# Kernel optimization log

Measured on AMD Instinct MI355X. Metric: run time of the kernel, lower is better.

## Reference

```python
import jax, jax.numpy as jnp
import numpy as np

BS, N, HEADS, DIN, DOUT = 512, 128, 8, 64, 64


def setup_inputs() -> dict:
    key = jax.random.key(0)
    k1, k2, k3, k4, k5 = jax.random.split(key, 5)
    h = jax.random.normal(k1, (BS, N, DIN), dtype=jnp.float32)
    w = jax.random.normal(k2, (HEADS, DIN, DOUT), dtype=jnp.float32) * 0.1
    a_src = jax.random.normal(k3, (HEADS, DOUT, 1), dtype=jnp.float32) * 0.1
    a_dst = jax.random.normal(k4, (HEADS, DOUT, 1), dtype=jnp.float32) * 0.1
    bias = jnp.zeros((DOUT,), dtype=jnp.float32)
    # sparse random adjacency with self-loops so every softmax row is valid
    adj = jax.random.uniform(k5, (BS, N, N)) < 0.05
    adj = adj | jnp.eye(N, dtype=bool)[None, :, :]
    return {"h": h, "adj": adj, "w": w, "a_src": a_src, "a_dst": a_dst, "bias": bias}


def reference(h, adj, w, a_src, a_dst, bias):
    # h: [b, n, i]; w: [H, i, o] -> h_prime: [b, H, n, o]
    h_prime = jnp.einsum('bni,hio->bhno', h, w)
    t = jnp.tanh(h_prime)
    attn_src = jnp.einsum('bhno,ho->bhn', t, a_src[..., 0])  # [b, H, n]
    attn_dst = jnp.einsum('bhno,ho->bhn', t, a_dst[..., 0])  # [b, H, n]
    # attn[b,h,i,j] = src[b,h,i] + dst[b,h,j]
    attn = attn_src[..., :, None] + attn_dst[..., None, :]
    attn = jax.nn.leaky_relu(attn, negative_slope=0.2)
    attn = jnp.where(adj[:, None, :, :], attn, -jnp.inf)
    attn = jax.nn.softmax(attn, axis=-1)
    out = jnp.einsum('bhij,bhjo->bhio', attn, h_prime)
    return out + bias
```

## Files before the change

### kernel.cpp

```cpp
#include <hip/hip_runtime.h>

#define BSZ 512
#define NN 128
#define HEADS 8
#define DIN 64
#define DOUT 64

typedef __bf16 bf16x8 __attribute__((ext_vector_type(8)));
typedef float floatx4 __attribute__((ext_vector_type(4)));

static __device__ __forceinline__ unsigned short f2bf(float f) {
    __bf16 b = (__bf16)f;
    return __builtin_bit_cast(unsigned short, b);
}
static __device__ __forceinline__ bf16x8 ld_frag(const unsigned short* p) {
    uint4 r = *reinterpret_cast<const uint4*>(p);
    return __builtin_bit_cast(bf16x8, r);
}

__global__ __launch_bounds__(512) void prep(
    const int* __restrict__ adj, const float* __restrict__ w,
    unsigned int* __restrict__ msk, unsigned short* __restrict__ wT, int do_w)
{
    const int b = blockIdx.x;
    const int t = threadIdx.x;
    const int* ap = adj + (size_t)b * NN * NN + (t >> 2) * NN + (t & 3) * 32;
    unsigned int m = 0;
    #pragma unroll
    for (int q = 0; q < 8; ++q) {
        int4 v = *reinterpret_cast<const int4*>(ap + q * 4);
        m |= (v.x != 0 ? (1u << (4 * q + 0)) : 0u)
           | (v.y != 0 ? (1u << (4 * q + 1)) : 0u)
           | (v.z != 0 ? (1u << (4 * q + 2)) : 0u)
           | (v.w != 0 ? (1u << (4 * q + 3)) : 0u);
    }
    msk[b * 512 + t] = m;

    if (do_w && b < HEADS) {
        const float* wg = w + b * DIN * DOUT;
        const int o = t >> 3, k0 = (t & 7) * 8;
        unsigned int u[4];
        #pragma unroll
        for (int p = 0; p < 4; ++p) {
            float f0 = wg[(k0 + 2 * p) * DOUT + o];
            float f1 = wg[(k0 + 2 * p + 1) * DOUT + o];
            u[p] = f2bf(f0) | ((unsigned int)f2bf(f1) << 16);
        }
        *reinterpret_cast<uint4*>(&wT[b * DOUT * DIN + o * DIN + k0]) =
            make_uint4(u[0], u[1], u[2], u[3]);
    }
}

__global__ __launch_bounds__(512, 8) void gat_fwd(
    const float* __restrict__ hin,
    const unsigned int* __restrict__ mskg,
    const unsigned short* __restrict__ wTg,
    const float* __restrict__ w,
    const float* __restrict__ a_src,
    const float* __restrict__ a_dst,
    const float* __restrict__ bias,
    float* __restrict__ out)
{
    __shared__ __attribute__((aligned(16))) unsigned short hpT[DOUT * NN];
    __shared__ __attribute__((aligned(16))) float s_src[NN];
    __shared__ __attribute__((aligned(16))) float s_dst[NN];

    const int bid  = blockIdx.x;
    const int b    = bid >> 3;
    const int hd   = bid & 7;
    const int tid  = threadIdx.x;
    const int lane = tid & 63;
    const int wv   = tid >> 6;
    const int lg   = lane >> 4;
    const int lm   = lane & 15;
    const int n0   = wv * 16;

    const float* hb = hin + (size_t)b * NN * DIN;
    bf16x8 hA[2];
    #pragma unroll
    for (int kt = 0; kt < 2; ++kt) {
        const float* p = hb + (n0 + lm) * DIN + kt * 32 + lg * 8;
        float4 v0 = *reinterpret_cast<const float4*>(p);
        float4 v1 = *reinterpret_cast<const float4*>(p + 4);
        bf16x8 a;
        a[0] = (__bf16)v0.x; a[1] = (__bf16)v0.y; a[2] = (__bf16)v0.z; a[3] = (__bf16)v0.w;
        a[4] = (__bf16)v1.x; a[5] = (__bf16)v1.y; a[6] = (__bf16)v1.z; a[7] = (__bf16)v1.w;
        hA[kt] = a;
    }
    const uint4 mr = *reinterpret_cast<const uint4*>(&mskg[(size_t)b * 512 + (n0 + lm) * 4]);
    unsigned int mwv[4] = {mr.x, mr.y, mr.z, mr.w};

    floatx4 acc[4] = {floatx4{0,0,0,0}, floatx4{0,0,0,0}, floatx4{0,0,0,0}, floatx4{0,0,0,0}};
    if (wTg) {
        const unsigned short* wt = wTg + hd * DOUT * DIN;
        #pragma unroll
        for (int kt = 0; kt < 2; ++kt) {
            #pragma unroll
            for (int nt = 0; nt < 4; ++nt) {
                bf16x8 bfr = ld_frag(&wt[(nt * 16 + lm) * DIN + kt * 32 + lg * 8]);
                acc[nt] = __builtin_amdgcn_mfma_f32_16x16x32_bf16(hA[kt], bfr, acc[nt], 0, 0, 0);
            }
        }
    } else {
        const float* wg = w + hd * DIN * DOUT;
        #pragma unroll
        for (int kt = 0; kt < 2; ++kt) {
            #pragma unroll
            for (int nt = 0; nt < 4; ++nt) {
                const float* wp = wg + (kt * 32 + lg * 8) * DOUT + nt * 16 + lm;
                bf16x8 bfr;
                #pragma unroll
                for (int q = 0; q < 8; ++q) bfr[q] = (__bf16)wp[q * DOUT];
                acc[nt] = __builtin_amdgcn_mfma_f32_16x16x32_bf16(hA[kt], bfr, acc[nt], 0, 0, 0);
            }
        }
    }
    const float* asp = a_src + hd * DOUT;
    const float* adp = a_dst + hd * DOUT;
    float ps[4] = {0, 0, 0, 0}, pd[4] = {0, 0, 0, 0};
    #pragma unroll
    for (int nt = 0; nt < 4; ++nt) {
        const int o = nt * 16 + lm;
        const float as = asp[o], ad = adp[o];
        #pragma unroll
        for (int r = 0; r < 4; ++r) {
            const float v = acc[nt][r];
            const float ex = __expf(2.f * v);
            const float t = 1.f - 2.f / (ex + 1.f);
            ps[r] = fmaf(t, as, ps[r]);
            pd[r] = fmaf(t, ad, pd[r]);
        }
        const int jb = n0 + lg * 4;
        unsigned int u01 = f2bf(acc[nt][0]) | ((unsigned int)f2bf(acc[nt][1]) << 16);
        unsigned int u23 = f2bf(acc[nt][2]) | ((unsigned int)f2bf(acc[nt][3]) << 16);
        const int base = (o * 128 + jb) ^ ((o & 7) << 3);
        *reinterpret_cast<unsigned int*>(&hpT[base])     = u01;
        *reinterpret_cast<unsigned int*>(&hpT[base + 2]) = u23;
    }
    #pragma unroll
    for (int r = 0; r < 4; ++r) {
        #pragma unroll
        for (int m = 1; m <= 8; m <<= 1) {
            ps[r] += __shfl_xor(ps[r], m);
            pd[r] += __shfl_xor(pd[r], m);
        }
    }
    if (lm == 0) {
        #pragma unroll
        for (int r = 0; r < 4; ++r) {
            s_src[n0 + lg * 4 + r] = ps[r];
            s_dst[n0 + lg * 4 + r] = pd[r];
        }
    }
    __syncthreads();

    const int i = n0 + lm;
    const float si = s_src[i];

    float sum = 0.f;
    bf16x8 pf[4];
    #pragma unroll
    for (int kt = 0; kt < 4; ++kt) {
        unsigned long long d01 = 0ull, d23 = 0ull;
        unsigned int byte = (mwv[kt] >> (lg * 8)) & 0xffu;
        while (byte) {
            const int q = __builtin_ctz(byte); byte &= byte - 1;
            const float x = si + s_dst[kt * 32 + lg * 8 + q];
            const float xl = fmaxf(x, 0.f) + 0.2f * fminf(x, 0.f);
            const float e = __expf(xl);
            const __bf16 eb = (__bf16)e;
            sum += (float)eb;
            const unsigned long long v =
                (unsigned long long)__builtin_bit_cast(unsigned short, eb) << ((q & 3) * 16);
            if (q < 4) d01 |= v; else d23 |= v;
        }
        const uint4 ui = make_uint4((unsigned)d01, (unsigned)(d01 >> 32),
                                    (unsigned)d23, (unsigned)(d23 >> 32));
        pf[kt] = __builtin_bit_cast(bf16x8, ui);
    }
    sum += __shfl_xor(sum, 16);
    sum += __shfl_xor(sum, 32);
    const float inv = 1.f / sum;

    floatx4 oacc[4] = {floatx4{0,0,0,0}, floatx4{0,0,0,0}, floatx4{0,0,0,0}, floatx4{0,0,0,0}};
    #pragma unroll
    for (int kt = 0; kt < 4; ++kt) {
        #pragma unroll
        for (int nt = 0; nt < 4; ++nt) {
            const int o = nt * 16 + lm;
            bf16x8 bfr = ld_frag(&hpT[(o * 128 + kt * 32 + lg * 8) ^ ((o & 7) << 3)]);
            oacc[nt] = __builtin_amdgcn_mfma_f32_16x16x32_bf16(bfr, pf[kt], oacc[nt], 0, 0, 0);
        }
    }
    float* outr = out + (((size_t)b * HEADS + hd) * NN + i) * DOUT;
    #pragma unroll
    for (int nt = 0; nt < 4; ++nt) {
        const float4 bv = *reinterpret_cast<const float4*>(&bias[nt * 16 + lg * 4]);
        floatx4 st;
        st[0] = fmaf(oacc[nt][0], inv, bv.x);
        st[1] = fmaf(oacc[nt][1], inv, bv.y);
        st[2] = fmaf(oacc[nt][2], inv, bv.z);
        st[3] = fmaf(oacc[nt][3], inv, bv.w);
        __builtin_nontemporal_store(st, reinterpret_cast<floatx4*>(&outr[nt * 16 + lg * 4]));
    }
}

extern "C" void kernel_launch(void* const* d_in, const int* in_sizes, int n_in,
                              void* d_out, int out_size, void* d_ws, size_t ws_size,
                              hipStream_t stream) {
    (void)in_sizes; (void)n_in; (void)out_size;
    const float* h     = (const float*)d_in[0];
    const int*   adj   = (const int*)d_in[1];
    const float* w     = (const float*)d_in[2];
    const float* a_src = (const float*)d_in[3];
    const float* a_dst = (const float*)d_in[4];
    const float* bias  = (const float*)d_in[5];
    float* out = (float*)d_out;

    unsigned int* msk = (unsigned int*)d_ws;
    const size_t MSK_BYTES = (size_t)BSZ * 512 * 4;
    unsigned short* wT = nullptr;
    const bool use_wt = ws_size >= MSK_BYTES + (size_t)HEADS * DOUT * DIN * 2;
    if (use_wt) wT = (unsigned short*)((char*)d_ws + MSK_BYTES);

    prep<<<dim3(BSZ), dim3(512), 0, stream>>>(adj, w, msk, wT, use_wt ? 1 : 0);
    gat_fwd<<<dim3(BSZ * HEADS), dim3(512), 0, stream>>>(h, msk, wT, w, a_src, a_dst, bias, out);
}
```

Before: 78.80 us.

## Pre-convert h to bf16 in prep, use exp2/rcp intrinsics, drop nontemporal stores

The prep kernel now also converts h to bf16 in workspace, so each of the 8 head blocks per batch loads half the bytes and skips the per-element conversion. The tanh and softmax exponentials use hardware exp2 with log2e folded into the stored scores, and divisions become rcp intrinsics. Output stores switch from nontemporal to regular stores. These changes add an extra write and read of a 8 MB bf16 copy of h, depend on the workspace being large enough, and slightly lower the accuracy of the transcendentals.

```diff
diff --git a/kernel.cpp b/kernel.cpp
--- a/kernel.cpp
+++ b/kernel.cpp
@@ -9,6 +9,8 @@
 typedef __bf16 bf16x8 __attribute__((ext_vector_type(8)));
 typedef float floatx4 __attribute__((ext_vector_type(4)));
 
+#define L2E 1.44269504f
+
 static __device__ __forceinline__ unsigned short f2bf(float f) {
     __bf16 b = (__bf16)f;
     return __builtin_bit_cast(unsigned short, b);
@@ -20,7 +22,9 @@
 
 __global__ __launch_bounds__(512) void prep(
     const int* __restrict__ adj, const float* __restrict__ w,
-    unsigned int* __restrict__ msk, unsigned short* __restrict__ wT, int do_w)
+    const float* __restrict__ h,
+    unsigned int* __restrict__ msk, unsigned short* __restrict__ wT,
+    unsigned short* __restrict__ hbf, int do_w, int do_h)
 {
     const int b = blockIdx.x;
     const int t = threadIdx.x;
@@ -36,6 +40,19 @@
     }
     msk[b * 512 + t] = m;
 
+    if (do_h) {
+        const float* hp = h + (size_t)b * NN * DIN + t * 16;
+        unsigned int u[8];
+        #pragma unroll
+        for (int p = 0; p < 4; ++p) {
+            float4 v = *reinterpret_cast<const float4*>(hp + 4 * p);
+            u[2 * p]     = f2bf(v.x) | ((unsigned int)f2bf(v.y) << 16);
+            u[2 * p + 1] = f2bf(v.z) | ((unsigned int)f2bf(v.w) << 16);
+        }
+        unsigned short* dst = hbf + (size_t)b * NN * DIN + t * 16;
+        *reinterpret_cast<uint4*>(dst)     = make_uint4(u[0], u[1], u[2], u[3]);
+        *reinterpret_cast<uint4*>(dst + 8) = make_uint4(u[4], u[5], u[6], u[7]);
+    }
     if (do_w && b < HEADS) {
         const float* wg = w + b * DIN * DOUT;
         const int o = t >> 3, k0 = (t & 7) * 8;
@@ -53,6 +70,7 @@
 
 __global__ __launch_bounds__(512, 8) void gat_fwd(
     const float* __restrict__ hin,
+    const unsigned short* __restrict__ hbfg,
     const unsigned int* __restrict__ mskg,
     const unsigned short* __restrict__ wTg,
     const float* __restrict__ w,
@@ -75,17 +93,23 @@
     const int lm   = lane & 15;
     const int n0   = wv * 16;
 
-    const float* hb = hin + (size_t)b * NN * DIN;
     bf16x8 hA[2];
-    #pragma unroll
-    for (int kt = 0; kt < 2; ++kt) {
-        const float* p = hb + (n0 + lm) * DIN + kt * 32 + lg * 8;
-        float4 v0 = *reinterpret_cast<const float4*>(p);
-        float4 v1 = *reinterpret_cast<const float4*>(p + 4);
-        bf16x8 a;
-        a[0] = (__bf16)v0.x; a[1] = (__bf16)v0.y; a[2] = (__bf16)v0.z; a[3] = (__bf16)v0.w;
-        a[4] = (__bf16)v1.x; a[5] = (__bf16)v1.y; a[6] = (__bf16)v1.z; a[7] = (__bf16)v1.w;
-        hA[kt] = a;
+    if (hbfg) {
+        const unsigned short* hq = hbfg + ((size_t)b * NN + n0 + lm) * DIN + lg * 8;
+        hA[0] = ld_frag(hq);
+        hA[1] = ld_frag(hq + 32);
+    } else {
+        const float* hb = hin + (size_t)b * NN * DIN;
+        #pragma unroll
+        for (int kt = 0; kt < 2; ++kt) {
+            const float* p = hb + (n0 + lm) * DIN + kt * 32 + lg * 8;
+            float4 v0 = *reinterpret_cast<const float4*>(p);
+            float4 v1 = *reinterpret_cast<const float4*>(p + 4);
+            bf16x8 a;
+            a[0] = (__bf16)v0.x; a[1] = (__bf16)v0.y; a[2] = (__bf16)v0.z; a[3] = (__bf16)v0.w;
+            a[4] = (__bf16)v1.x; a[5] = (__bf16)v1.y; a[6] = (__bf16)v1.z; a[7] = (__bf16)v1.w;
+            hA[kt] = a;
+        }
     }
     const uint4 mr = *reinterpret_cast<const uint4*>(&mskg[(size_t)b * 512 + (n0 + lm) * 4]);
     unsigned int mwv[4] = {mr.x, mr.y, mr.z, mr.w};
@@ -125,8 +149,8 @@
         #pragma unroll
         for (int r = 0; r < 4; ++r) {
             const float v = acc[nt][r];
-            const float ex = __expf(2.f * v);
-            const float t = 1.f - 2.f / (ex + 1.f);
+            const float e2 = __builtin_amdgcn_exp2f(v * (2.f * L2E));
+            const float t  = 1.f - 2.f * __builtin_amdgcn_rcpf(e2 + 1.f);
             ps[r] = fmaf(t, as, ps[r]);
             pd[r] = fmaf(t, ad, pd[r]);
         }
@@ -148,8 +172,8 @@
     if (lm == 0) {
         #pragma unroll
         for (int r = 0; r < 4; ++r) {
-            s_src[n0 + lg * 4 + r] = ps[r];
-            s_dst[n0 + lg * 4 + r] = pd[r];
+            s_src[n0 + lg * 4 + r] = ps[r] * L2E;
+            s_dst[n0 + lg * 4 + r] = pd[r] * L2E;
         }
     }
     __syncthreads();
@@ -167,7 +191,7 @@
             const int q = __builtin_ctz(byte); byte &= byte - 1;
             const float x = si + s_dst[kt * 32 + lg * 8 + q];
             const float xl = fmaxf(x, 0.f) + 0.2f * fminf(x, 0.f);
-            const float e = __expf(xl);
+            const float e = __builtin_amdgcn_exp2f(xl);
             const __bf16 eb = (__bf16)e;
             sum += (float)eb;
             const unsigned long long v =
@@ -180,7 +204,7 @@
     }
     sum += __shfl_xor(sum, 16);
     sum += __shfl_xor(sum, 32);
-    const float inv = 1.f / sum;
+    const float inv = __builtin_amdgcn_rcpf(sum);
 
     floatx4 oacc[4] = {floatx4{0,0,0,0}, floatx4{0,0,0,0}, floatx4{0,0,0,0}, floatx4{0,0,0,0}};
     #pragma unroll
@@ -201,7 +225,7 @@
         st[1] = fmaf(oacc[nt][1], inv, bv.y);
         st[2] = fmaf(oacc[nt][2], inv, bv.z);
         st[3] = fmaf(oacc[nt][3], inv, bv.w);
-        __builtin_nontemporal_store(st, reinterpret_cast<floatx4*>(&outr[nt * 16 + lg * 4]));
+        *reinterpret_cast<floatx4*>(&outr[nt * 16 + lg * 4]) = st;
     }
 }
 
@@ -217,12 +241,20 @@
     const float* bias  = (const float*)d_in[5];
     float* out = (float*)d_out;
 
-    unsigned int* msk = (unsigned int*)d_ws;
     const size_t MSK_BYTES = (size_t)BSZ * 512 * 4;
-    unsigned short* wT = nullptr;
-    const bool use_wt = ws_size >= MSK_BYTES + (size_t)HEADS * DOUT * DIN * 2;
-    if (use_wt) wT = (unsigned short*)((char*)d_ws + MSK_BYTES);
-
-    prep<<<dim3(BSZ), dim3(512), 0, stream>>>(adj, w, msk, wT, use_wt ? 1 : 0);
-    gat_fwd<<<dim3(BSZ * HEADS), dim3(512), 0, stream>>>(h, msk, wT, w, a_src, a_dst, bias, out);
-}
+    const size_t WT_BYTES  = (size_t)HEADS * DOUT * DIN * 2;
+    const size_t HBF_BYTES = (size_t)BSZ * NN * DIN * 2;
+
+    unsigned int*   msk = (unsigned int*)d_ws;
+    unsigned short* wT  = nullptr;
+    unsigned short* hbf = nullptr;
+    const bool use_wt = ws_size >= MSK_BYTES + WT_BYTES;
+    const bool use_h  = ws_size >= MSK_BYTES + WT_BYTES + HBF_BYTES;
+    if (use_wt) wT  = (unsigned short*)((char*)d_ws + MSK_BYTES);
+    if (use_h)  hbf = (unsigned short*)((char*)d_ws + MSK_BYTES + WT_BYTES);
+
+    prep<<<dim3(BSZ), dim3(512), 0, stream>>>(adj, w, h, msk, wT, hbf,
+                                              use_wt ? 1 : 0, use_h ? 1 : 0);
+    gat_fwd<<<dim3(BSZ * HEADS), dim3(512), 0, stream>>>(h, hbf, msk, wT, w,
+                                                         a_src, a_dst, bias, out);
+}
```

Measured after the change: 75.41 us. -4.3%, faster.
